# Performance work log

Hardware: AMD Instinct MI355X
Metric: run time of the kernel (lower is better)

Reference implementation:

```python
import jax, jax.numpy as jnp
import numpy as np

B, D, E, H = 8192, 2048, 8, 128

def setup_inputs() -> dict:
    key = jax.random.key(0)
    ks = jax.random.split(key, 9)
    s_d = 1.0 / np.sqrt(D)
    s_h = 1.0 / np.sqrt(H)
    return {
        "x": jax.random.normal(ks[0], (B, D), dtype=jnp.float32),
        "gate_w": jax.random.normal(ks[1], (D, E), dtype=jnp.float32) * s_d,
        "gate_b": jnp.zeros((E,), dtype=jnp.float32),
        "W1": jax.random.normal(ks[2], (E, D, H), dtype=jnp.float32) * s_d,
        "b1": jnp.zeros((E, H), dtype=jnp.float32),
        "W2": jax.random.normal(ks[3], (E, H, H), dtype=jnp.float32) * s_h,
        "b2": jnp.zeros((E, H), dtype=jnp.float32),
        "W3": jax.random.normal(ks[4], (E, H, D), dtype=jnp.float32) * s_h,
        "b3": jnp.zeros((E, D), dtype=jnp.float32),
    }

def reference(x, gate_w, gate_b, W1, b1, W2, b2, W3, b3):
    # Adaptive gate: softmax over experts
    gates = jax.nn.softmax(x @ gate_w + gate_b, axis=1)          # [B, E]
    # All experts as one batched (grouped) GEMM over the expert axis.
    h1 = jax.nn.silu(jnp.einsum('bd,edh->ebh', x, W1) + b1[:, None, :])   # [E, B, H]
    h2 = jax.nn.silu(jnp.einsum('ebh,ehk->ebk', h1, W2) + b2[:, None, :]) # [E, B, H]
    y = jnp.einsum('ebh,ehd->ebd', h2, W3) + b3[:, None, :]               # [E, B, D]
    # Gate-weighted sum over experts (fused reduction, no [B,E,D] stack kept)
    out = jnp.einsum('be,ebd->bd', gates, y)                     # [B, D]
    return out
```

## Files before the change

### kernel.cpp

```cpp
#include <hip/hip_runtime.h>


typedef __attribute__((ext_vector_type(8))) short short8;
typedef __attribute__((ext_vector_type(4))) short bf16x4;
typedef __attribute__((ext_vector_type(4))) float f32x4;

#define B_SZ 8192
#define D_SZ 2048
#define E_SZ 8
#define H_SZ 128

__device__ __forceinline__ short f2bf(float f) {
  unsigned u = __builtin_bit_cast(unsigned, f);
  unsigned r = (u + 0x7fffu + ((u >> 16) & 1u)) >> 16;
  return (short)r;
}

__device__ __forceinline__ float silu_f(float v) {
  return v / (1.f + __expf(-v));
}

__device__ __forceinline__ void gload_lds16(const void* g, void* l) {
  __builtin_amdgcn_global_load_lds(
      (const __attribute__((address_space(1))) void*)g,
      (__attribute__((address_space(3))) void*)l,
      16, 0, 0);
}

template<int NHT>
__device__ __forceinline__ void core128(const short* __restrict__ A,
                                        const short* __restrict__ B,
                                        short* lds, f32x4 acc[4][4])
{
  const int tid  = threadIdx.x;
  const int lane = tid & 63;
  const int wid  = tid >> 6;
  const int wr = wid >> 1, wc = wid & 1;
  const int lm = lane & 15, lk = lane >> 4;
  const int wl = (tid & ~63) * 8;

  auto STAGE = [&](int eta) {
    const size_t go = (size_t)(eta >> 1)*8192 + (size_t)(eta & 1)*4096;
    short* l = lds + (eta & 1)*8192;
    gload_lds16(A + go + tid*8,        l + wl);
    gload_lds16(A + go + 2048 + tid*8, l + 2048 + wl);
    gload_lds16(B + go + tid*8,        l + 4096 + wl);
    gload_lds16(B + go + 2048 + tid*8, l + 6144 + wl);
  };

  STAGE(0);
  __syncthreads();
  for (int eta = 0; eta < NHT; ++eta) {
    if (eta + 1 < NHT) STAGE(eta + 1);
    const short* la = lds + (eta & 1)*8192 + lk*1024 + (wr*64 + lm)*8;
    const short* lb = lds + (eta & 1)*8192 + 4096 + lk*1024 + (wc*64 + lm)*8;
    short8 av[4], bv[4];
    #pragma unroll
    for (int f = 0; f < 4; ++f) av[f] = *(const short8*)(la + f*128);
    #pragma unroll
    for (int f = 0; f < 4; ++f) bv[f] = *(const short8*)(lb + f*128);
    #pragma unroll
    for (int i = 0; i < 4; ++i)
      #pragma unroll
      for (int j = 0; j < 4; ++j)
        acc[i][j] = __builtin_amdgcn_mfma_f32_16x16x32_bf16(av[i], bv[j], acc[i][j], 0, 0, 0);
    __syncthreads();
  }
}

template<int NKT>
__device__ __forceinline__ void core64k(const short* __restrict__ A,
                                        const short* __restrict__ B,
                                        short* lds, f32x4 acc[4][4])
{
  const int tid  = threadIdx.x;
  const int lane = tid & 63;
  const int wid  = tid >> 6;
  const int wr = wid >> 1, wc = wid & 1;
  const int lm = lane & 15, lk = lane >> 4;
  const int wbase = tid & ~63;

  auto STAGE = [&](int kt) {
    const short* ga = A + (size_t)kt*8192;
    const short* gb = B + (size_t)kt*8192;
    short* la = lds + (kt & 1)*8192;
    short* lb = lds + 16384 + (kt & 1)*8192;
    #pragma unroll
    for (int q = 0; q < 4; ++q) {
      gload_lds16(ga + (q*256 + tid)*8, la + (q*256 + wbase)*8);
      gload_lds16(gb + (q*256 + tid)*8, lb + (q*256 + wbase)*8);
    }
  };

  STAGE(0);
  __syncthreads();
  for (int kt = 0; kt < NKT; ++kt) {
    if (kt + 1 < NKT) STAGE(kt + 1);
    const short* Ac = lds + (kt & 1)*8192;
    const short* Bc = lds + 16384 + (kt & 1)*8192;
    #pragma unroll
    for (int ks = 0; ks < 2; ++ks) {
      short8 av[4], bv[4];
      #pragma unroll
      for (int f = 0; f < 4; ++f)
        av[f] = *(const short8*)(Ac + (ks*4 + lk)*1024 + (wr*64 + f*16 + lm)*8);
      #pragma unroll
      for (int f = 0; f < 4; ++f)
        bv[f] = *(const short8*)(Bc + (ks*4 + lk)*1024 + (wc*64 + f*16 + lm)*8);
      #pragma unroll
      for (int i = 0; i < 4; ++i)
        #pragma unroll
        for (int j = 0; j < 4; ++j)
          acc[i][j] = __builtin_amdgcn_mfma_f32_16x16x32_bf16(av[i], bv[j], acc[i][j], 0, 0, 0);
    }
    __syncthreads();
  }
}

__global__ __launch_bounds__(256)
void k_cvt_gate(const float* __restrict__ x,  const float* __restrict__ W1,
                const float* __restrict__ W2, const float* __restrict__ W3,
                const float* __restrict__ gw, const float* __restrict__ gb,
                short* __restrict__ xf, short* __restrict__ w1f,
                short* __restrict__ w2f, short* __restrict__ w3f,
                float* __restrict__ gates)
{
  __shared__ short lt[8192];
  const int b = blockIdx.x;
  const int tid = threadIdx.x;

  if (b < 512) {
    const int lane = tid & 63, wid = tid >> 6;
    const int row0 = b*16 + wid*4;
    float acc[4][8] = {};
    #pragma unroll
    for (int it = 0; it < 8; ++it) {
      const int k = it*256 + lane*4;
      float4 xv[4];
      #pragma unroll
      for (int r = 0; r < 4; ++r)
        xv[r] = *(const float4*)(x + (size_t)(row0 + r)*2048 + k);
      float4 gv[4][2];
      #pragma unroll
      for (int d = 0; d < 4; ++d) {
        gv[d][0] = *(const float4*)(gw + (size_t)(k + d)*8);
        gv[d][1] = *(const float4*)(gw + (size_t)(k + d)*8 + 4);
      }
      #pragma unroll
      for (int r = 0; r < 4; ++r) {
        const float xr[4] = {xv[r].x, xv[r].y, xv[r].z, xv[r].w};
        #pragma unroll
        for (int d = 0; d < 4; ++d) {
          acc[r][0] += xr[d]*gv[d][0].x; acc[r][1] += xr[d]*gv[d][0].y;
          acc[r][2] += xr[d]*gv[d][0].z; acc[r][3] += xr[d]*gv[d][0].w;
          acc[r][4] += xr[d]*gv[d][1].x; acc[r][5] += xr[d]*gv[d][1].y;
          acc[r][6] += xr[d]*gv[d][1].z; acc[r][7] += xr[d]*gv[d][1].w;
        }
      }
    }
    #pragma unroll
    for (int r = 0; r < 4; ++r)
      #pragma unroll
      for (int e = 0; e < 8; ++e)
        #pragma unroll
        for (int d = 1; d < 64; d <<= 1)
          acc[r][e] += __shfl_xor(acc[r][e], d, 64);
    if (lane < 4) {
      float lg[8], mx = -1e30f;
      #pragma unroll
      for (int e = 0; e < 8; ++e) { lg[e] = acc[lane][e] + gb[e]; mx = fmaxf(mx, lg[e]); }
      float s = 0.f;
      #pragma unroll
      for (int e = 0; e < 8; ++e) { lg[e] = __expf(lg[e] - mx); s += lg[e]; }
      const float inv = 1.f / s;
      #pragma unroll
      for (int e = 0; e < 8; ++e) gates[(size_t)(row0 + lane)*8 + e] = lg[e] * inv;
    }
  } else if (b < 2560) {
    const int t = b - 512;
    const int bt = t >> 5, kt = t & 31;
    const float* xb = x + (size_t)bt*128*2048 + kt*64;
    #pragma unroll
    for (int u = 0; u < 8; ++u) {
      const int flat = u*1024 + tid*4;
      const int row = flat >> 6, kk = flat & 63;
      const float4 v = *(const float4*)(xb + (size_t)row*2048 + kk);
      const int kg = kk >> 3;
      bf16x4 o;
      o[0] = f2bf(v.x); o[1] = f2bf(v.y); o[2] = f2bf(v.z); o[3] = f2bf(v.w);
      const int s = (kg*1024 + row*8 + (kk & 7)) ^ ((kg & 7) << 3);
      *(bf16x4*)(lt + s) = o;
    }
    __syncthreads();
    short* dst = xf + (size_t)t*8192;
    #pragma unroll
    for (int u = 0; u < 4; ++u) {
      const int li = u*2048 + tid*8;
      const int kg = li >> 10;
      const int s = li ^ ((kg & 7) << 3);
      *(short8*)(dst + li) = *(const short8*)(lt + s);
    }
  } else {
    const int gi = (b - 2560)*256 + tid + 2097152;
    if (gi < 2097152 + 262144) {
      const int g = gi - 2097152;
      const int t = g >> 10, r = g & 1023;
      const int e = t >> 5, kt = t & 31;
      const int kg = r >> 7, p = r & 127;
      const int k0 = kt*64 + kg*8;
      short8 o;
      #pragma unroll
      for (int j = 0; j < 8; ++j)
        o[j] = f2bf(W1[(size_t)e*262144 + (size_t)(k0 + j)*128 + p]);
      *(short8*)(w1f + (size_t)g*8) = o;
    } else if (gi < 2097152 + 262144 + 16384) {
      const int g = gi - (2097152 + 262144);
      const int t = g >> 10, r = g & 1023;
      const int e = t >> 1, kt = t & 1;
      const int kg = r >> 7, p = r & 127;
      const int k0 = kt*64 + kg*8;
      short8 o;
      #pragma unroll
      for (int j = 0; j < 8; ++j)
        o[j] = f2bf(W2[(size_t)e*16384 + (size_t)(k0 + j)*128 + p]);
      *(short8*)(w2f + (size_t)g*8) = o;
    } else if (gi < 2637824) {
      const int g = gi - 2375680;
      const int t = g >> 10, r = g & 1023;
      const int nt = t >> 4, kt = t & 15;
      const int kg = r >> 7, p = r & 127;
      const int k0 = kt*64 + kg*8;
      short8 o;
      #pragma unroll
      for (int j = 0; j < 8; ++j) {
        const int k = k0 + j;
        o[j] = f2bf(W3[(size_t)(k >> 7)*262144 + (size_t)(k & 127)*2048 + nt*128 + p]);
      }
      *(short8*)(w3f + (size_t)g*8) = o;
    }
  }
}

__global__ __launch_bounds__(256, 2)
void k_gemm12f(const short* __restrict__ xf, const short* __restrict__ w1f,
               const short* __restrict__ w2f,
               const float* __restrict__ b1, const float* __restrict__ b2,
               const float* __restrict__ gates, short* __restrict__ h2gf)
{
  __shared__ short lds[32768];
  const int b = blockIdx.x;
  const int xcd = b & 7, idx = b >> 3;
  const int bt = xcd*8 + (idx & 7);
  const int e  = idx >> 3;

  f32x4 acc[4][4] = {};
  core64k<32>(xf  + (size_t)bt*32*8192,
              w1f + (size_t)e*32*8192,
              lds, acc);

  const int tid = threadIdx.x, lane = tid & 63, wid = tid >> 6;
  const int wr = wid >> 1, wc = wid & 1;
  const int lm = lane & 15, lk = lane >> 4, lr = lane >> 4;

  short8 bvAll[2][2][4];
  #pragma unroll
  for (int kt = 0; kt < 2; ++kt)
  #pragma unroll
  for (int ks = 0; ks < 2; ++ks)
  #pragma unroll
  for (int fn = 0; fn < 4; ++fn)
    bvAll[kt][ks][fn] = *(const short8*)(
        w2f + (size_t)e*16384 + kt*8192 + (ks*4 + lk)*1024
            + (wc*64 + fn*16 + lm)*8);

  float gv[4][4];
  #pragma unroll
  for (int fm = 0; fm < 4; ++fm)
  #pragma unroll
  for (int i = 0; i < 4; ++i)
    gv[fm][i] = gates[(size_t)(bt*128 + wr*64 + fm*16 + lr*4 + i)*8 + e];

  float b1v[4];
  #pragma unroll
  for (int fn = 0; fn < 4; ++fn) b1v[fn] = b1[e*H_SZ + wc*64 + fn*16 + lm];
  #pragma unroll
  for (int fm = 0; fm < 4; ++fm)
  #pragma unroll
  for (int i = 0; i < 4; ++i) {
    const int m = wr*64 + fm*16 + lr*4 + i;
    #pragma unroll
    for (int fn = 0; fn < 4; ++fn) {
      const int n = wc*64 + fn*16 + lm;
      const float v = silu_f(acc[fm][fn][i] + b1v[fn]);
      lds[(n >> 3)*1024 + m*8 + (n & 7)] = f2bf(v);
    }
  }
  __syncthreads();

  f32x4 acc2[4][4] = {};
  #pragma unroll
  for (int kt = 0; kt < 2; ++kt)
  #pragma unroll
  for (int ks = 0; ks < 2; ++ks) {
    short8 av[4];
    #pragma unroll
    for (int f = 0; f < 4; ++f)
      av[f] = *(const short8*)(lds + (kt*8 + ks*4 + lk)*1024 + (wr*64 + f*16 + lm)*8);
    #pragma unroll
    for (int i = 0; i < 4; ++i)
      #pragma unroll
      for (int j = 0; j < 4; ++j)
        acc2[i][j] = __builtin_amdgcn_mfma_f32_16x16x32_bf16(
            av[i], bvAll[kt][ks][j], acc2[i][j], 0, 0, 0);
  }
  __syncthreads();

  float b2v[4];
  #pragma unroll
  for (int fn = 0; fn < 4; ++fn) b2v[fn] = b2[e*H_SZ + wc*64 + fn*16 + lm];
  #pragma unroll
  for (int fm = 0; fm < 4; ++fm)
  #pragma unroll
  for (int i = 0; i < 4; ++i) {
    const int m = wr*64 + fm*16 + lr*4 + i;
    const float g = gv[fm][i];
    #pragma unroll
    for (int fn = 0; fn < 4; ++fn) {
      const int n = wc*64 + fn*16 + lm;
      const float v = silu_f(acc2[fm][fn][i] + b2v[fn]) * g;
      lds[(n >> 3)*1024 + m*8 + (n & 7)] = f2bf(v);
    }
  }
  __syncthreads();

  #pragma unroll
  for (int q = 0; q < 8; ++q) {
    const int li = q*2048 + tid*8;
    const int t2 = li >> 13, off = li & 8191;
    *(short8*)(h2gf + ((size_t)bt*16 + e*2 + t2)*8192 + off) =
        *(const short8*)(lds + li);
  }
}

__global__ __launch_bounds__(256, 4)
void k_gemm3(const short* __restrict__ h2gf, const short* __restrict__ w3f,
             const float* __restrict__ b3, const float* __restrict__ gates,
             float* __restrict__ out)
{
  __shared__ short lds[16384];
  const int b = blockIdx.x;
  const int xcd = b & 7, idx = b >> 3;
  const int bt = xcd*8 + (idx & 7);
  const int nt = idx >> 3;

  f32x4 acc[4][4] = {};
  core128<32>(h2gf + (size_t)bt*16*8192,
              w3f  + (size_t)nt*16*8192,
              lds, acc);

  const int tid = threadIdx.x, lane = tid & 63, wid = tid >> 6;
  const int wr = wid >> 1, wc = wid & 1, lm = lane & 15, lr = lane >> 4;
  float b3c[4][8];
  #pragma unroll
  for (int fn = 0; fn < 4; ++fn) {
    const int n = nt*128 + wc*64 + fn*16 + lm;
    #pragma unroll
    for (int e = 0; e < 8; ++e) b3c[fn][e] = b3[(size_t)e*D_SZ + n];
  }
  #pragma unroll
  for (int fm = 0; fm < 4; ++fm)
  #pragma unroll
  for (int i = 0; i < 4; ++i) {
    const int m = bt*128 + wr*64 + fm*16 + lr*4 + i;
    const float4 ga  = *(const float4*)(gates + (size_t)m*8);
    const float4 gbv = *(const float4*)(gates + (size_t)m*8 + 4);
    #pragma unroll
    for (int fn = 0; fn < 4; ++fn) {
      const int n = nt*128 + wc*64 + fn*16 + lm;
      const float bias = ga.x*b3c[fn][0] + ga.y*b3c[fn][1] + ga.z*b3c[fn][2] + ga.w*b3c[fn][3]
                       + gbv.x*b3c[fn][4] + gbv.y*b3c[fn][5] + gbv.z*b3c[fn][6] + gbv.w*b3c[fn][7];
      out[(size_t)m*D_SZ + n] = acc[fm][fn][i] + bias;
    }
  }
}

extern "C" void kernel_launch(void* const* d_in, const int* in_sizes, int n_in,
                              void* d_out, int out_size, void* d_ws, size_t ws_size,
                              hipStream_t stream)
{
  (void)in_sizes; (void)n_in; (void)out_size; (void)ws_size;
  const float* x  = (const float*)d_in[0];
  const float* gw = (const float*)d_in[1];
  const float* gb = (const float*)d_in[2];
  const float* W1 = (const float*)d_in[3];
  const float* b1 = (const float*)d_in[4];
  const float* W2 = (const float*)d_in[5];
  const float* b2 = (const float*)d_in[6];
  const float* W3 = (const float*)d_in[7];
  const float* b3 = (const float*)d_in[8];
  float* out = (float*)d_out;

  char* ws = (char*)d_ws;
  short* xf    = (short*)ws;  ws += (size_t)B_SZ*D_SZ*2;
  short* w1f   = (short*)ws;  ws += (size_t)E_SZ*D_SZ*H_SZ*2;
  short* w2f   = (short*)ws;  ws += (size_t)E_SZ*H_SZ*H_SZ*2;
  short* w3f   = (short*)ws;  ws += (size_t)E_SZ*H_SZ*D_SZ*2;
  float* gates = (float*)ws;  ws += (size_t)B_SZ*E_SZ*4;
  short* h2gf  = (short*)ws;  ws += (size_t)B_SZ*E_SZ*H_SZ*2;

  k_cvt_gate<<<dim3(4672), dim3(256), 0, stream>>>(x, W1, W2, W3, gw, gb,
                                                   xf, w1f, w2f, w3f, gates);
  k_gemm12f <<<dim3(512),  dim3(256), 0, stream>>>(xf, w1f, w2f, b1, b2, gates, h2gf);
  k_gemm3   <<<dim3(1024), dim3(256), 0, stream>>>(h2gf, w3f, b3, gates, out);
}
```

Measured before the change: 132.6 us.

## Fuse gate logit computation into x bf16 conversion blocks with atomic accumulation

Removes the separate gate-GEMV blocks, which re-read all of x, and computes partial gate logits inside the x-to-bf16 conversion blocks that already load x. Each block reduces partial logits over its 64-column slice with wave shuffles and atomically adds them into a zeroed gates buffer. Softmax is deferred to the consumers, so both GEMM kernels recompute it per row from the raw logits. The cost is a memset, many float atomics (about 32 per logit), extra shuffles in the conversion path, and redundant softmax work in the epilogues.

```diff
diff --git a/kernel.cpp b/kernel.cpp
--- a/kernel.cpp
+++ b/kernel.cpp
@@ -25,6 +25,20 @@
       (const __attribute__((address_space(1))) void*)g,
       (__attribute__((address_space(3))) void*)l,
       16, 0, 0);
+}
+
+__device__ __forceinline__ void softmax8(const float* __restrict__ logits,
+                                         const float* __restrict__ gbv,
+                                         float* __restrict__ out) {
+  float lg[8], mx = -1e30f;
+  #pragma unroll
+  for (int e = 0; e < 8; ++e) { lg[e] = logits[e] + gbv[e]; mx = fmaxf(mx, lg[e]); }
+  float s = 0.f;
+  #pragma unroll
+  for (int e = 0; e < 8; ++e) { lg[e] = __expf(lg[e] - mx); s += lg[e]; }
+  const float inv = 1.f / s;
+  #pragma unroll
+  for (int e = 0; e < 8; ++e) out[e] = lg[e] * inv;
 }
 
 template<int NHT>
@@ -120,7 +134,7 @@
 __global__ __launch_bounds__(256)
 void k_cvt_gate(const float* __restrict__ x,  const float* __restrict__ W1,
                 const float* __restrict__ W2, const float* __restrict__ W3,
-                const float* __restrict__ gw, const float* __restrict__ gb,
+                const float* __restrict__ gw,
                 short* __restrict__ xf, short* __restrict__ w1f,
                 short* __restrict__ w2f, short* __restrict__ w3f,
                 float* __restrict__ gates)
@@ -129,57 +143,20 @@
   const int b = blockIdx.x;
   const int tid = threadIdx.x;
 
-  if (b < 512) {
-    const int lane = tid & 63, wid = tid >> 6;
-    const int row0 = b*16 + wid*4;
-    float acc[4][8] = {};
-    #pragma unroll
-    for (int it = 0; it < 8; ++it) {
-      const int k = it*256 + lane*4;
-      float4 xv[4];
-      #pragma unroll
-      for (int r = 0; r < 4; ++r)
-        xv[r] = *(const float4*)(x + (size_t)(row0 + r)*2048 + k);
-      float4 gv[4][2];
-      #pragma unroll
-      for (int d = 0; d < 4; ++d) {
-        gv[d][0] = *(const float4*)(gw + (size_t)(k + d)*8);
-        gv[d][1] = *(const float4*)(gw + (size_t)(k + d)*8 + 4);
-      }
-      #pragma unroll
-      for (int r = 0; r < 4; ++r) {
-        const float xr[4] = {xv[r].x, xv[r].y, xv[r].z, xv[r].w};
-        #pragma unroll
-        for (int d = 0; d < 4; ++d) {
-          acc[r][0] += xr[d]*gv[d][0].x; acc[r][1] += xr[d]*gv[d][0].y;
-          acc[r][2] += xr[d]*gv[d][0].z; acc[r][3] += xr[d]*gv[d][0].w;
-          acc[r][4] += xr[d]*gv[d][1].x; acc[r][5] += xr[d]*gv[d][1].y;
-          acc[r][6] += xr[d]*gv[d][1].z; acc[r][7] += xr[d]*gv[d][1].w;
-        }
-      }
-    }
-    #pragma unroll
-    for (int r = 0; r < 4; ++r)
-      #pragma unroll
-      for (int e = 0; e < 8; ++e)
-        #pragma unroll
-        for (int d = 1; d < 64; d <<= 1)
-          acc[r][e] += __shfl_xor(acc[r][e], d, 64);
-    if (lane < 4) {
-      float lg[8], mx = -1e30f;
-      #pragma unroll
-      for (int e = 0; e < 8; ++e) { lg[e] = acc[lane][e] + gb[e]; mx = fmaxf(mx, lg[e]); }
-      float s = 0.f;
-      #pragma unroll
-      for (int e = 0; e < 8; ++e) { lg[e] = __expf(lg[e] - mx); s += lg[e]; }
-      const float inv = 1.f / s;
-      #pragma unroll
-      for (int e = 0; e < 8; ++e) gates[(size_t)(row0 + lane)*8 + e] = lg[e] * inv;
-    }
-  } else if (b < 2560) {
-    const int t = b - 512;
-    const int bt = t >> 5, kt = t & 31;
+  if (b < 2048) {
+    const int bt = b >> 5, kt = b & 31;
     const float* xb = x + (size_t)bt*128*2048 + kt*64;
+    const int lane = tid & 63;
+
+    float g8[4][8];
+    #pragma unroll
+    for (int d = 0; d < 4; ++d) {
+      const float4 a = *(const float4*)(gw + (size_t)(kt*64 + (tid & 15)*4 + d)*8);
+      const float4 c = *(const float4*)(gw + (size_t)(kt*64 + (tid & 15)*4 + d)*8 + 4);
+      g8[d][0]=a.x; g8[d][1]=a.y; g8[d][2]=a.z; g8[d][3]=a.w;
+      g8[d][4]=c.x; g8[d][5]=c.y; g8[d][6]=c.z; g8[d][7]=c.w;
+    }
+
     #pragma unroll
     for (int u = 0; u < 8; ++u) {
       const int flat = u*1024 + tid*4;
@@ -190,9 +167,24 @@
       o[0] = f2bf(v.x); o[1] = f2bf(v.y); o[2] = f2bf(v.z); o[3] = f2bf(v.w);
       const int s = (kg*1024 + row*8 + (kk & 7)) ^ ((kg & 7) << 3);
       *(bf16x4*)(lt + s) = o;
+      float pa[8];
+      #pragma unroll
+      for (int e = 0; e < 8; ++e)
+        pa[e] = v.x*g8[0][e] + v.y*g8[1][e] + v.z*g8[2][e] + v.w*g8[3][e];
+      #pragma unroll
+      for (int e = 0; e < 8; ++e) {
+        #pragma unroll
+        for (int d = 1; d < 16; d <<= 1)
+          pa[e] += __shfl_xor(pa[e], d, 64);
+      }
+      if ((lane & 15) == 0) {
+        float* gdst = gates + (size_t)(bt*128 + row)*8;
+        #pragma unroll
+        for (int e = 0; e < 8; ++e) atomicAdd(gdst + e, pa[e]);
+      }
     }
     __syncthreads();
-    short* dst = xf + (size_t)t*8192;
+    short* dst = xf + (size_t)b*8192;
     #pragma unroll
     for (int u = 0; u < 4; ++u) {
       const int li = u*2048 + tid*8;
@@ -201,7 +193,7 @@
       *(short8*)(dst + li) = *(const short8*)(lt + s);
     }
   } else {
-    const int gi = (b - 2560)*256 + tid + 2097152;
+    const int gi = (b - 2048)*256 + tid + 2097152;
     if (gi < 2097152 + 262144) {
       const int g = gi - 2097152;
       const int t = g >> 10, r = g & 1023;
@@ -245,7 +237,8 @@
 void k_gemm12f(const short* __restrict__ xf, const short* __restrict__ w1f,
                const short* __restrict__ w2f,
                const float* __restrict__ b1, const float* __restrict__ b2,
-               const float* __restrict__ gates, short* __restrict__ h2gf)
+               const float* __restrict__ gates, const float* __restrict__ gb,
+               short* __restrict__ h2gf)
 {
   __shared__ short lds[32768];
   const int b = blockIdx.x;
@@ -273,12 +266,23 @@
         w2f + (size_t)e*16384 + kt*8192 + (ks*4 + lk)*1024
             + (wc*64 + fn*16 + lm)*8);
 
+  float gbv[8];
+  #pragma unroll
+  for (int q = 0; q < 8; ++q) gbv[q] = gb[q];
   float gv[4][4];
   #pragma unroll
   for (int fm = 0; fm < 4; ++fm)
   #pragma unroll
-  for (int i = 0; i < 4; ++i)
-    gv[fm][i] = gates[(size_t)(bt*128 + wr*64 + fm*16 + lr*4 + i)*8 + e];
+  for (int i = 0; i < 4; ++i) {
+    const int row = bt*128 + wr*64 + fm*16 + lr*4 + i;
+    float lg[8], sm[8];
+    const float4 l0 = *(const float4*)(gates + (size_t)row*8);
+    const float4 l1 = *(const float4*)(gates + (size_t)row*8 + 4);
+    lg[0]=l0.x; lg[1]=l0.y; lg[2]=l0.z; lg[3]=l0.w;
+    lg[4]=l1.x; lg[5]=l1.y; lg[6]=l1.z; lg[7]=l1.w;
+    softmax8(lg, gbv, sm);
+    gv[fm][i] = sm[e];
+  }
 
   float b1v[4];
   #pragma unroll
@@ -345,7 +349,7 @@
 __global__ __launch_bounds__(256, 4)
 void k_gemm3(const short* __restrict__ h2gf, const short* __restrict__ w3f,
              const float* __restrict__ b3, const float* __restrict__ gates,
-             float* __restrict__ out)
+             const float* __restrict__ gb, float* __restrict__ out)
 {
   __shared__ short lds[16384];
   const int b = blockIdx.x;
@@ -367,18 +371,26 @@
     #pragma unroll
     for (int e = 0; e < 8; ++e) b3c[fn][e] = b3[(size_t)e*D_SZ + n];
   }
+  float gbv[8];
+  #pragma unroll
+  for (int q = 0; q < 8; ++q) gbv[q] = gb[q];
   #pragma unroll
   for (int fm = 0; fm < 4; ++fm)
   #pragma unroll
   for (int i = 0; i < 4; ++i) {
     const int m = bt*128 + wr*64 + fm*16 + lr*4 + i;
-    const float4 ga  = *(const float4*)(gates + (size_t)m*8);
-    const float4 gbv = *(const float4*)(gates + (size_t)m*8 + 4);
+    float lg[8], sm[8];
+    const float4 l0 = *(const float4*)(gates + (size_t)m*8);
+    const float4 l1 = *(const float4*)(gates + (size_t)m*8 + 4);
+    lg[0]=l0.x; lg[1]=l0.y; lg[2]=l0.z; lg[3]=l0.w;
+    lg[4]=l1.x; lg[5]=l1.y; lg[6]=l1.z; lg[7]=l1.w;
+    softmax8(lg, gbv, sm);
     #pragma unroll
     for (int fn = 0; fn < 4; ++fn) {
       const int n = nt*128 + wc*64 + fn*16 + lm;
-      const float bias = ga.x*b3c[fn][0] + ga.y*b3c[fn][1] + ga.z*b3c[fn][2] + ga.w*b3c[fn][3]
-                       + gbv.x*b3c[fn][4] + gbv.y*b3c[fn][5] + gbv.z*b3c[fn][6] + gbv.w*b3c[fn][7];
+      float bias = 0.f;
+      #pragma unroll
+      for (int e = 0; e < 8; ++e) bias += sm[e] * b3c[fn][e];
       out[(size_t)m*D_SZ + n] = acc[fm][fn][i] + bias;
     }
   }
@@ -408,8 +420,10 @@
   float* gates = (float*)ws;  ws += (size_t)B_SZ*E_SZ*4;
   short* h2gf  = (short*)ws;  ws += (size_t)B_SZ*E_SZ*H_SZ*2;
 
-  k_cvt_gate<<<dim3(4672), dim3(256), 0, stream>>>(x, W1, W2, W3, gw, gb,
+  hipMemsetAsync(gates, 0, (size_t)B_SZ*E_SZ*4, stream);
+  k_cvt_gate<<<dim3(4160), dim3(256), 0, stream>>>(x, W1, W2, W3, gw,
                                                    xf, w1f, w2f, w3f, gates);
-  k_gemm12f <<<dim3(512),  dim3(256), 0, stream>>>(xf, w1f, w2f, b1, b2, gates, h2gf);
-  k_gemm3   <<<dim3(1024), dim3(256), 0, stream>>>(h2gf, w3f, b3, gates, out);
-}
+  k_gemm12f <<<dim3(512),  dim3(256), 0, stream>>>(xf, w1f, w2f, b1, b2,
+                                                   gates, gb, h2gf);
+  k_gemm3   <<<dim3(1024), dim3(256), 0, stream>>>(h2gf, w3f, b3, gates, gb, out);
+}
```

After: 222.0 us. 67.4% more time.
